# Optimization experiments

Measured on AMD Instinct MI355X. Metric: run time of the kernel, lower is better.

## Reference

```python
import jax, jax.numpy as jnp
import numpy as np

B = 2
N_PER = 100000
M_PER = 27648
C = 32
Z, Y, X = 21, 400, 352
MAX_RANGE = (2, 2, 2)
RADIUS = 8.0
NSAMPLE = 16
VS = np.array([0.2, 0.2, 0.4], np.float32)  # voxel size (x, y, z)


def setup_inputs() -> dict:
    key = jax.random.key(0)
    ks = jax.random.split(key, 6)
    N = B * N_PER
    M = B * M_PER
    space = jnp.array([X * VS[0], Y * VS[1], Z * VS[2]], jnp.float32)
    xyz = jax.random.uniform(ks[0], (N, 3), jnp.float32) * space
    zc = jax.random.randint(ks[1], (M,), 0, Z)
    yc = jax.random.randint(ks[2], (M,), 0, Y)
    xc = jax.random.randint(ks[3], (M,), 0, X)
    bq = jnp.repeat(jnp.arange(B, dtype=jnp.int32), M_PER)
    new_coords = jnp.stack([bq, zc, yc, xc], 1).astype(jnp.int32)
    new_xyz = jnp.stack([(xc + 0.5) * VS[0], (yc + 0.5) * VS[1], (zc + 0.5) * VS[2]], 1).astype(jnp.float32)
    features = jax.random.normal(ks[4], (N, C), jnp.float32)
    raw = jax.random.randint(ks[5], (B, Z, Y, X), -N_PER, N_PER)
    offs = (jnp.arange(B) * N_PER)[:, None, None, None]
    voxel2point_indices = jnp.where(raw < 0, -1, raw + offs).astype(jnp.int32)
    xyz_batch_cnt = jnp.full((B,), N_PER, jnp.int32)
    new_xyz_batch_cnt = jnp.full((B,), M_PER, jnp.int32)
    return dict(new_coords=new_coords, xyz=xyz, xyz_batch_cnt=xyz_batch_cnt,
                new_xyz=new_xyz, new_xyz_batch_cnt=new_xyz_batch_cnt,
                features=features, voxel2point_indices=voxel2point_indices)


def _voxel_query(xyz, new_xyz, new_coords, point_indices):
    """Vectorized equivalent of the CUDA voxel_query kernel.
    Returns (idx (M, nsample) int32 global point indices, empty_ball_mask (M,) bool)."""
    zr, yr, xr = MAX_RANGE
    _, Zg, Yg, Xg = point_indices.shape
    M = new_coords.shape[0]
    dz, dy, dx = jnp.meshgrid(jnp.arange(-zr, zr + 1), jnp.arange(-yr, yr + 1),
                              jnp.arange(-xr, xr + 1), indexing='ij')
    offs = jnp.stack([dz.ravel(), dy.ravel(), dx.ravel()], 1)  # (K,3) in CUDA loop order z,y,x
    nb = new_coords[:, None, 1:4] + offs[None]                 # (M,K,3) candidate voxels
    lim = jnp.array([Zg, Yg, Xg])
    inb = jnp.all((nb >= 0) & (nb < lim), -1)                  # (M,K) in-bounds
    nbc = jnp.clip(nb, 0, lim - 1)
    b = new_coords[:, 0]
    pidx = point_indices[b[:, None], nbc[..., 0], nbc[..., 1], nbc[..., 2]]  # (M,K)
    valid = inb & (pidx >= 0)
    pts = xyz[jnp.maximum(pidx, 0)]                            # (M,K,3)
    d2 = jnp.sum((pts - new_xyz[:, None, :]) ** 2, -1)
    valid = valid & (d2 < RADIUS * RADIUS)
    cnt = jnp.minimum(valid.sum(-1), NSAMPLE)                  # (M,)
    # assign each valid candidate its in-order slot; overflow/invalid go to dump column
    slot = jnp.cumsum(valid, -1) - 1
    slot = jnp.where(valid & (slot < NSAMPLE), slot, NSAMPLE)
    rows = jnp.arange(M)[:, None]
    idx = jnp.zeros((M, NSAMPLE + 1), jnp.int32).at[rows, slot].set(pidx)[:, :NSAMPLE]
    first = idx[:, 0]  # CUDA pre-fills all slots with first found index
    idx = jnp.where(jnp.arange(NSAMPLE)[None, :] < cnt[:, None], idx, first[:, None])
    empty = cnt == 0
    idx = jnp.where(empty[:, None], 0, idx)
    return idx, empty


def reference(new_coords, xyz, xyz_batch_cnt, new_xyz, new_xyz_batch_cnt, features, voxel2point_indices):
    idx, empty = _voxel_query(xyz, new_xyz, new_coords, voxel2point_indices)
    # global -> batch-relative (as in the torch loop), empty balls -> 0 of their batch
    xyz_offs = jnp.concatenate([jnp.zeros(1, jnp.int32), jnp.cumsum(xyz_batch_cnt)[:-1].astype(jnp.int32)])
    qb = new_coords[:, 0]
    idx_rel = jnp.where(empty[:, None], 0, idx - xyz_offs[qb][:, None])
    # grouping_operation (stack version): gather with batch offset added back
    gidx = idx_rel + xyz_offs[qb][:, None]                     # (M, nsample) global indices
    grouped_xyz = jnp.transpose(xyz[gidx], (0, 2, 1))          # (M, 3, nsample)
    grouped_features = jnp.transpose(features[gidx], (0, 2, 1))  # (M, C, nsample)
    return grouped_features, grouped_xyz, empty
```

## Files before the change

kernel.cpp:

```cpp
#include <hip/hip_runtime.h>


constexpr int ZG = 21;
constexpr int YG = 400;
constexpr int XG = 352;
constexpr int NS = 16;
constexpr int CF = 32;
constexpr float R2 = 64.0f;

typedef float v4f __attribute__((ext_vector_type(4)));

struct QState {
    int  cnt;
    int  boff;
    int  gfin;
};

__global__ __launch_bounds__(256) void vqg_kernel(
    const int*   __restrict__ new_coords,
    const float* __restrict__ xyz,
    const int*   __restrict__ xyz_batch_cnt,
    const float* __restrict__ new_xyz,
    const float* __restrict__ features,
    const int*   __restrict__ v2p,
    float* __restrict__ out_feat,
    float* __restrict__ out_xyz,
    float* __restrict__ out_empty,
    int M)
{
    const int lane = threadIdx.x & 63;
    const int w    = (blockIdx.x * 256 + threadIdx.x) >> 6;
    const int m0   = w * 2;
    const int m1   = m0 + 1;
    if (m0 >= M) return;
    const bool has1 = (m1 < M);

    const int4 qc0 = *reinterpret_cast<const int4*>(new_coords + (size_t)m0 * 4);
    const int4 qc1 = has1 ? *reinterpret_cast<const int4*>(new_coords + (size_t)m1 * 4) : qc0;
    const float qx0 = new_xyz[m0 * 3 + 0], qy0 = new_xyz[m0 * 3 + 1], qz0 = new_xyz[m0 * 3 + 2];
    const float qx1 = has1 ? new_xyz[m1 * 3 + 0] : 0.f;
    const float qy1 = has1 ? new_xyz[m1 * 3 + 1] : 0.f;
    const float qz1 = has1 ? new_xyz[m1 * 3 + 2] : 0.f;

    int boff0 = 0, boff1 = 0;
    for (int i = 0; i < qc0.x; ++i) boff0 += xyz_batch_cnt[i];
    for (int i = 0; i < qc1.x; ++i) boff1 += xyz_batch_cnt[i];

    const int n0 = lane;
    const int n1 = 64 + lane;
    const int dz0 = n0 / 25 - 2, dy0 = (n0 / 5) % 5 - 2, dx0 = n0 % 5 - 2;
    const int dz1 = n1 / 25 - 2, dy1 = (n1 / 5) % 5 - 2, dx1 = n1 % 5 - 2;
    const bool in1 = (n1 < 125);

    const int* __restrict__ gb0 = v2p + (size_t)qc0.x * (ZG * YG * XG);
    const int* __restrict__ gb1 = v2p + (size_t)qc1.x * (ZG * YG * XG);

    int pa0 = -1, pa1 = -1, pb0 = -1, pb1 = -1;
    {
        const int z = qc0.y + dz0, y = qc0.z + dy0, x = qc0.w + dx0;
        if ((unsigned)z < (unsigned)ZG && (unsigned)y < (unsigned)YG && (unsigned)x < (unsigned)XG)
            pa0 = gb0[((size_t)z * YG + y) * XG + x];
    }
    {
        const int z = qc0.y + dz1, y = qc0.z + dy1, x = qc0.w + dx1;
        if (in1 && (unsigned)z < (unsigned)ZG && (unsigned)y < (unsigned)YG && (unsigned)x < (unsigned)XG)
            pa1 = gb0[((size_t)z * YG + y) * XG + x];
    }
    if (has1) {
        const int z = qc1.y + dz0, y = qc1.z + dy0, x = qc1.w + dx0;
        if ((unsigned)z < (unsigned)ZG && (unsigned)y < (unsigned)YG && (unsigned)x < (unsigned)XG)
            pb0 = gb1[((size_t)z * YG + y) * XG + x];
    }
    if (has1) {
        const int z = qc1.y + dz1, y = qc1.z + dy1, x = qc1.w + dx1;
        if (in1 && (unsigned)z < (unsigned)ZG && (unsigned)y < (unsigned)YG && (unsigned)x < (unsigned)XG)
            pb1 = gb1[((size_t)z * YG + y) * XG + x];
    }

    float a0x = 0, a0y = 0, a0z = 0, a1x = 0, a1y = 0, a1z = 0;
    float b0x = 0, b0y = 0, b0z = 0, b1x = 0, b1y = 0, b1z = 0;
    if (pa0 >= 0) { const float* p = xyz + (size_t)pa0 * 3; a0x = p[0]; a0y = p[1]; a0z = p[2]; }
    if (pa1 >= 0) { const float* p = xyz + (size_t)pa1 * 3; a1x = p[0]; a1y = p[1]; a1z = p[2]; }
    if (pb0 >= 0) { const float* p = xyz + (size_t)pb0 * 3; b0x = p[0]; b0y = p[1]; b0z = p[2]; }
    if (pb1 >= 0) { const float* p = xyz + (size_t)pb1 * 3; b1x = p[0]; b1y = p[1]; b1z = p[2]; }

    bool va0 = false, va1 = false, vb0 = false, vb1 = false;
    if (pa0 >= 0) {
        const float dx = a0x - qx0, dy = a0y - qy0, dz = a0z - qz0;
        va0 = __fadd_rn(__fadd_rn(__fmul_rn(dx, dx), __fmul_rn(dy, dy)), __fmul_rn(dz, dz)) < R2;
    }
    if (pa1 >= 0) {
        const float dx = a1x - qx0, dy = a1y - qy0, dz = a1z - qz0;
        va1 = __fadd_rn(__fadd_rn(__fmul_rn(dx, dx), __fmul_rn(dy, dy)), __fmul_rn(dz, dz)) < R2;
    }
    if (pb0 >= 0) {
        const float dx = b0x - qx1, dy = b0y - qy1, dz = b0z - qz1;
        vb0 = __fadd_rn(__fadd_rn(__fmul_rn(dx, dx), __fmul_rn(dy, dy)), __fmul_rn(dz, dz)) < R2;
    }
    if (pb1 >= 0) {
        const float dx = b1x - qx1, dy = b1y - qy1, dz = b1z - qz1;
        vb1 = __fadd_rn(__fadd_rn(__fmul_rn(dx, dx), __fmul_rn(dy, dy)), __fmul_rn(dz, dz)) < R2;
    }

    const unsigned long long below = (1ull << lane) - 1ull;
    const int junk = (16 + (lane & 31)) << 2;

    int cnt0, gfin0;
    {
        const unsigned long long bal0 = __ballot(va0);
        const unsigned long long bal1 = __ballot(va1);
        const int c0   = (int)__popcll(bal0);
        cnt0 = c0 + (int)__popcll(bal1);
        const int pos0 = (int)__popcll(bal0 & below);
        const int pos1 = c0 + (int)__popcll(bal1 & below);
        const int addr0 = (va0 && pos0 < NS) ? (pos0 << 2) : junk;
        const int addr1 = (va1 && pos1 < NS) ? (pos1 << 2) : junk;
        const int perm0 = __builtin_amdgcn_ds_permute(addr0, pa0);
        const int perm1 = __builtin_amdgcn_ds_permute(addr1, pa1);
        const int sel   = (lane < c0) ? perm0 : perm1;
        const int first = __shfl(sel, 0);
        const int c16   = cnt0 < NS ? cnt0 : NS;
        gfin0 = (cnt0 == 0) ? boff0 : (((lane & 15) < c16) ? sel : first);
    }
    int cnt1 = 0, gfin1 = 0;
    if (has1) {
        const unsigned long long bal0 = __ballot(vb0);
        const unsigned long long bal1 = __ballot(vb1);
        const int c0   = (int)__popcll(bal0);
        cnt1 = c0 + (int)__popcll(bal1);
        const int pos0 = (int)__popcll(bal0 & below);
        const int pos1 = c0 + (int)__popcll(bal1 & below);
        const int addr0 = (vb0 && pos0 < NS) ? (pos0 << 2) : junk;
        const int addr1 = (vb1 && pos1 < NS) ? (pos1 << 2) : junk;
        const int perm0 = __builtin_amdgcn_ds_permute(addr0, pb0);
        const int perm1 = __builtin_amdgcn_ds_permute(addr1, pb1);
        const int sel   = (lane < c0) ? perm0 : perm1;
        const int first = __shfl(sel, 0);
        const int c16   = cnt1 < NS ? cnt1 : NS;
        gfin1 = (cnt1 == 0) ? boff1 : (((lane & 15) < c16) ? sel : first);
    }

    const int s0lane = (lane & 3) << 2;
    const int a_r0 = __shfl(gfin0, s0lane + 0);
    const int a_r1 = __shfl(gfin0, s0lane + 1);
    const int a_r2 = __shfl(gfin0, s0lane + 2);
    const int a_r3 = __shfl(gfin0, s0lane + 3);
    const int b_r0 = __shfl(gfin1, s0lane + 0);
    const int b_r1 = __shfl(gfin1, s0lane + 1);
    const int b_r2 = __shfl(gfin1, s0lane + 2);
    const int b_r3 = __shfl(gfin1, s0lane + 3);

    {
        const int s = lane & 15;
        const int d = lane >> 4;
        if (lane < 48) {
            const int row = __shfl(gfin0, s);
            __builtin_nontemporal_store(xyz[(size_t)row * 3 + d],
                                        out_xyz + (size_t)m0 * 48 + d * 16 + s);
        }
        if (lane == 0)
            __builtin_nontemporal_store(cnt0 == 0 ? 1.0f : 0.0f, out_empty + m0);
        if (has1) {
            if (lane < 48) {
                const int row = __shfl(gfin1, s);
                __builtin_nontemporal_store(xyz[(size_t)row * 3 + d],
                                            out_xyz + (size_t)m1 * 48 + d * 16 + s);
            }
            if (lane == 0)
                __builtin_nontemporal_store(cnt1 == 0 ? 1.0f : 0.0f, out_empty + m1);
        }
    }

    float* __restrict__ of0 = out_feat + (size_t)m0 * (CF * NS);
    float* __restrict__ of1 = out_feat + (size_t)m1 * (CF * NS);
    #pragma unroll
    for (int k = 0; k < 2; ++k) {
        const int c = k * 16 + (lane >> 2);
        v4f v;
        v[0] = features[(size_t)a_r0 * CF + c];
        v[1] = features[(size_t)a_r1 * CF + c];
        v[2] = features[(size_t)a_r2 * CF + c];
        v[3] = features[(size_t)a_r3 * CF + c];
        __builtin_nontemporal_store(v, reinterpret_cast<v4f*>(of0 + k * 256 + (lane << 2)));
    }
    if (has1) {
        #pragma unroll
        for (int k = 0; k < 2; ++k) {
            const int c = k * 16 + (lane >> 2);
            v4f v;
            v[0] = features[(size_t)b_r0 * CF + c];
            v[1] = features[(size_t)b_r1 * CF + c];
            v[2] = features[(size_t)b_r2 * CF + c];
            v[3] = features[(size_t)b_r3 * CF + c];
            __builtin_nontemporal_store(v, reinterpret_cast<v4f*>(of1 + k * 256 + (lane << 2)));
        }
    }
}

extern "C" void kernel_launch(void* const* d_in, const int* in_sizes, int n_in,
                              void* d_out, int out_size, void* d_ws, size_t ws_size,
                              hipStream_t stream) {
    const int*   new_coords    = (const int*)d_in[0];
    const float* xyz           = (const float*)d_in[1];
    const int*   xyz_batch_cnt = (const int*)d_in[2];
    const float* new_xyz       = (const float*)d_in[3];
    const float* features      = (const float*)d_in[5];
    const int*   v2p           = (const int*)d_in[6];

    const int M = in_sizes[0] / 4;

    float* out_feat  = (float*)d_out;
    float* out_xyz   = out_feat + (size_t)M * CF * NS;
    float* out_empty = out_xyz + (size_t)M * 3 * NS;

    const int waves  = (M + 1) / 2;
    const int blocks = (waves + 3) / 4;
    vqg_kernel<<<blocks, 256, 0, stream>>>(
        new_coords, xyz, xyz_batch_cnt, new_xyz, features, v2p,
        out_feat, out_xyz, out_empty, M);
}
```

Before: 53.43 us.

## Convert to persistent grid-stride waves with software-prefetched voxel lookups

Switches from one wave per query pair to a fixed grid of 8192 waves that loop over pairs with a stride. While the current pair is processed, the next pair's descriptors and its voxel-grid indices are loaded, so the dependent gather chain overlaps with the previous pair's work. The aim is to hide the latency of the v2p -> xyz -> features load chain, at the cost of more live registers and less wave-level parallelism, since there are about 27.6k pairs for 8192 waves.

```diff
diff --git a/kernel.cpp b/kernel.cpp
--- a/kernel.cpp
+++ b/kernel.cpp
@@ -10,10 +10,11 @@
 
 typedef float v4f __attribute__((ext_vector_type(4)));
 
-struct QState {
-    int  cnt;
-    int  boff;
-    int  gfin;
+struct PairDesc {
+    int4  qc0, qc1;
+    float qx0, qy0, qz0, qx1, qy1, qz1;
+    int   boff0, boff1;
+    bool  has1;
 };
 
 __global__ __launch_bounds__(256) void vqg_kernel(
@@ -26,174 +27,199 @@
     float* __restrict__ out_feat,
     float* __restrict__ out_xyz,
     float* __restrict__ out_empty,
-    int M)
+    int M, int nwaves)
 {
     const int lane = threadIdx.x & 63;
     const int w    = (blockIdx.x * 256 + threadIdx.x) >> 6;
-    const int m0   = w * 2;
-    const int m1   = m0 + 1;
-    if (m0 >= M) return;
-    const bool has1 = (m1 < M);
-
-    const int4 qc0 = *reinterpret_cast<const int4*>(new_coords + (size_t)m0 * 4);
-    const int4 qc1 = has1 ? *reinterpret_cast<const int4*>(new_coords + (size_t)m1 * 4) : qc0;
-    const float qx0 = new_xyz[m0 * 3 + 0], qy0 = new_xyz[m0 * 3 + 1], qz0 = new_xyz[m0 * 3 + 2];
-    const float qx1 = has1 ? new_xyz[m1 * 3 + 0] : 0.f;
-    const float qy1 = has1 ? new_xyz[m1 * 3 + 1] : 0.f;
-    const float qz1 = has1 ? new_xyz[m1 * 3 + 2] : 0.f;
-
-    int boff0 = 0, boff1 = 0;
-    for (int i = 0; i < qc0.x; ++i) boff0 += xyz_batch_cnt[i];
-    for (int i = 0; i < qc1.x; ++i) boff1 += xyz_batch_cnt[i];
-
-    const int n0 = lane;
+    const int npairs = (M + 1) / 2;
+    int slot = w;
+    if (slot >= npairs) return;
+
     const int n1 = 64 + lane;
-    const int dz0 = n0 / 25 - 2, dy0 = (n0 / 5) % 5 - 2, dx0 = n0 % 5 - 2;
-    const int dz1 = n1 / 25 - 2, dy1 = (n1 / 5) % 5 - 2, dx1 = n1 % 5 - 2;
+    const int dz0 = lane / 25 - 2, dy0 = (lane / 5) % 5 - 2, dx0 = lane % 5 - 2;
+    const int dz1 = n1 / 25 - 2,   dy1 = (n1 / 5) % 5 - 2,   dx1 = n1 % 5 - 2;
     const bool in1 = (n1 < 125);
-
-    const int* __restrict__ gb0 = v2p + (size_t)qc0.x * (ZG * YG * XG);
-    const int* __restrict__ gb1 = v2p + (size_t)qc1.x * (ZG * YG * XG);
-
-    int pa0 = -1, pa1 = -1, pb0 = -1, pb1 = -1;
-    {
-        const int z = qc0.y + dz0, y = qc0.z + dy0, x = qc0.w + dx0;
-        if ((unsigned)z < (unsigned)ZG && (unsigned)y < (unsigned)YG && (unsigned)x < (unsigned)XG)
-            pa0 = gb0[((size_t)z * YG + y) * XG + x];
-    }
-    {
-        const int z = qc0.y + dz1, y = qc0.z + dy1, x = qc0.w + dx1;
-        if (in1 && (unsigned)z < (unsigned)ZG && (unsigned)y < (unsigned)YG && (unsigned)x < (unsigned)XG)
-            pa1 = gb0[((size_t)z * YG + y) * XG + x];
-    }
-    if (has1) {
-        const int z = qc1.y + dz0, y = qc1.z + dy0, x = qc1.w + dx0;
-        if ((unsigned)z < (unsigned)ZG && (unsigned)y < (unsigned)YG && (unsigned)x < (unsigned)XG)
-            pb0 = gb1[((size_t)z * YG + y) * XG + x];
-    }
-    if (has1) {
-        const int z = qc1.y + dz1, y = qc1.z + dy1, x = qc1.w + dx1;
-        if (in1 && (unsigned)z < (unsigned)ZG && (unsigned)y < (unsigned)YG && (unsigned)x < (unsigned)XG)
-            pb1 = gb1[((size_t)z * YG + y) * XG + x];
-    }
-
-    float a0x = 0, a0y = 0, a0z = 0, a1x = 0, a1y = 0, a1z = 0;
-    float b0x = 0, b0y = 0, b0z = 0, b1x = 0, b1y = 0, b1z = 0;
-    if (pa0 >= 0) { const float* p = xyz + (size_t)pa0 * 3; a0x = p[0]; a0y = p[1]; a0z = p[2]; }
-    if (pa1 >= 0) { const float* p = xyz + (size_t)pa1 * 3; a1x = p[0]; a1y = p[1]; a1z = p[2]; }
-    if (pb0 >= 0) { const float* p = xyz + (size_t)pb0 * 3; b0x = p[0]; b0y = p[1]; b0z = p[2]; }
-    if (pb1 >= 0) { const float* p = xyz + (size_t)pb1 * 3; b1x = p[0]; b1y = p[1]; b1z = p[2]; }
-
-    bool va0 = false, va1 = false, vb0 = false, vb1 = false;
-    if (pa0 >= 0) {
-        const float dx = a0x - qx0, dy = a0y - qy0, dz = a0z - qz0;
-        va0 = __fadd_rn(__fadd_rn(__fmul_rn(dx, dx), __fmul_rn(dy, dy)), __fmul_rn(dz, dz)) < R2;
-    }
-    if (pa1 >= 0) {
-        const float dx = a1x - qx0, dy = a1y - qy0, dz = a1z - qz0;
-        va1 = __fadd_rn(__fadd_rn(__fmul_rn(dx, dx), __fmul_rn(dy, dy)), __fmul_rn(dz, dz)) < R2;
-    }
-    if (pb0 >= 0) {
-        const float dx = b0x - qx1, dy = b0y - qy1, dz = b0z - qz1;
-        vb0 = __fadd_rn(__fadd_rn(__fmul_rn(dx, dx), __fmul_rn(dy, dy)), __fmul_rn(dz, dz)) < R2;
-    }
-    if (pb1 >= 0) {
-        const float dx = b1x - qx1, dy = b1y - qy1, dz = b1z - qz1;
-        vb1 = __fadd_rn(__fadd_rn(__fmul_rn(dx, dx), __fmul_rn(dy, dy)), __fmul_rn(dz, dz)) < R2;
-    }
-
     const unsigned long long below = (1ull << lane) - 1ull;
     const int junk = (16 + (lane & 31)) << 2;
 
-    int cnt0, gfin0;
-    {
-        const unsigned long long bal0 = __ballot(va0);
-        const unsigned long long bal1 = __ballot(va1);
-        const int c0   = (int)__popcll(bal0);
-        cnt0 = c0 + (int)__popcll(bal1);
-        const int pos0 = (int)__popcll(bal0 & below);
-        const int pos1 = c0 + (int)__popcll(bal1 & below);
-        const int addr0 = (va0 && pos0 < NS) ? (pos0 << 2) : junk;
-        const int addr1 = (va1 && pos1 < NS) ? (pos1 << 2) : junk;
-        const int perm0 = __builtin_amdgcn_ds_permute(addr0, pa0);
-        const int perm1 = __builtin_amdgcn_ds_permute(addr1, pa1);
-        const int sel   = (lane < c0) ? perm0 : perm1;
-        const int first = __shfl(sel, 0);
-        const int c16   = cnt0 < NS ? cnt0 : NS;
-        gfin0 = (cnt0 == 0) ? boff0 : (((lane & 15) < c16) ? sel : first);
-    }
-    int cnt1 = 0, gfin1 = 0;
-    if (has1) {
-        const unsigned long long bal0 = __ballot(vb0);
-        const unsigned long long bal1 = __ballot(vb1);
-        const int c0   = (int)__popcll(bal0);
-        cnt1 = c0 + (int)__popcll(bal1);
-        const int pos0 = (int)__popcll(bal0 & below);
-        const int pos1 = c0 + (int)__popcll(bal1 & below);
-        const int addr0 = (vb0 && pos0 < NS) ? (pos0 << 2) : junk;
-        const int addr1 = (vb1 && pos1 < NS) ? (pos1 << 2) : junk;
-        const int perm0 = __builtin_amdgcn_ds_permute(addr0, pb0);
-        const int perm1 = __builtin_amdgcn_ds_permute(addr1, pb1);
-        const int sel   = (lane < c0) ? perm0 : perm1;
-        const int first = __shfl(sel, 0);
-        const int c16   = cnt1 < NS ? cnt1 : NS;
-        gfin1 = (cnt1 == 0) ? boff1 : (((lane & 15) < c16) ? sel : first);
-    }
-
-    const int s0lane = (lane & 3) << 2;
-    const int a_r0 = __shfl(gfin0, s0lane + 0);
-    const int a_r1 = __shfl(gfin0, s0lane + 1);
-    const int a_r2 = __shfl(gfin0, s0lane + 2);
-    const int a_r3 = __shfl(gfin0, s0lane + 3);
-    const int b_r0 = __shfl(gfin1, s0lane + 0);
-    const int b_r1 = __shfl(gfin1, s0lane + 1);
-    const int b_r2 = __shfl(gfin1, s0lane + 2);
-    const int b_r3 = __shfl(gfin1, s0lane + 3);
-
-    {
-        const int s = lane & 15;
-        const int d = lane >> 4;
-        if (lane < 48) {
-            const int row = __shfl(gfin0, s);
-            __builtin_nontemporal_store(xyz[(size_t)row * 3 + d],
-                                        out_xyz + (size_t)m0 * 48 + d * 16 + s);
-        }
-        if (lane == 0)
-            __builtin_nontemporal_store(cnt0 == 0 ? 1.0f : 0.0f, out_empty + m0);
+    auto load_desc = [&](int s, PairDesc& d) {
+        const int m0 = s * 2, m1 = m0 + 1;
+        d.has1 = (m1 < M);
+        d.qc0 = *reinterpret_cast<const int4*>(new_coords + (size_t)m0 * 4);
+        d.qc1 = d.has1 ? *reinterpret_cast<const int4*>(new_coords + (size_t)m1 * 4) : d.qc0;
+        d.qx0 = new_xyz[m0 * 3 + 0]; d.qy0 = new_xyz[m0 * 3 + 1]; d.qz0 = new_xyz[m0 * 3 + 2];
+        d.qx1 = d.has1 ? new_xyz[m1 * 3 + 0] : 0.f;
+        d.qy1 = d.has1 ? new_xyz[m1 * 3 + 1] : 0.f;
+        d.qz1 = d.has1 ? new_xyz[m1 * 3 + 2] : 0.f;
+        int b0 = 0, b1 = 0;
+        for (int i = 0; i < d.qc0.x; ++i) b0 += xyz_batch_cnt[i];
+        for (int i = 0; i < d.qc1.x; ++i) b1 += xyz_batch_cnt[i];
+        d.boff0 = b0; d.boff1 = b1;
+    };
+    auto load_v2p = [&](const PairDesc& d, int& pa0, int& pa1, int& pb0, int& pb1) {
+        const int* __restrict__ gb0 = v2p + (size_t)d.qc0.x * (ZG * YG * XG);
+        const int* __restrict__ gb1 = v2p + (size_t)d.qc1.x * (ZG * YG * XG);
+        pa0 = -1; pa1 = -1; pb0 = -1; pb1 = -1;
+        {
+            const int z = d.qc0.y + dz0, y = d.qc0.z + dy0, x = d.qc0.w + dx0;
+            if ((unsigned)z < (unsigned)ZG && (unsigned)y < (unsigned)YG && (unsigned)x < (unsigned)XG)
+                pa0 = gb0[((size_t)z * YG + y) * XG + x];
+        }
+        {
+            const int z = d.qc0.y + dz1, y = d.qc0.z + dy1, x = d.qc0.w + dx1;
+            if (in1 && (unsigned)z < (unsigned)ZG && (unsigned)y < (unsigned)YG && (unsigned)x < (unsigned)XG)
+                pa1 = gb0[((size_t)z * YG + y) * XG + x];
+        }
+        if (d.has1) {
+            const int z = d.qc1.y + dz0, y = d.qc1.z + dy0, x = d.qc1.w + dx0;
+            if ((unsigned)z < (unsigned)ZG && (unsigned)y < (unsigned)YG && (unsigned)x < (unsigned)XG)
+                pb0 = gb1[((size_t)z * YG + y) * XG + x];
+        }
+        if (d.has1) {
+            const int z = d.qc1.y + dz1, y = d.qc1.z + dy1, x = d.qc1.w + dx1;
+            if (in1 && (unsigned)z < (unsigned)ZG && (unsigned)y < (unsigned)YG && (unsigned)x < (unsigned)XG)
+                pb1 = gb1[((size_t)z * YG + y) * XG + x];
+        }
+    };
+
+    PairDesc cur;
+    int pa0, pa1, pb0, pb1;
+    load_desc(slot, cur);
+    load_v2p(cur, pa0, pa1, pb0, pb1);
+
+    for (;;) {
+        const int m0 = slot * 2, m1 = m0 + 1;
+        const bool has1 = cur.has1;
+
+        float a0x = 0, a0y = 0, a0z = 0, a1x = 0, a1y = 0, a1z = 0;
+        float b0x = 0, b0y = 0, b0z = 0, b1x = 0, b1y = 0, b1z = 0;
+        if (pa0 >= 0) { const float* p = xyz + (size_t)pa0 * 3; a0x = p[0]; a0y = p[1]; a0z = p[2]; }
+        if (pa1 >= 0) { const float* p = xyz + (size_t)pa1 * 3; a1x = p[0]; a1y = p[1]; a1z = p[2]; }
+        if (pb0 >= 0) { const float* p = xyz + (size_t)pb0 * 3; b0x = p[0]; b0y = p[1]; b0z = p[2]; }
+        if (pb1 >= 0) { const float* p = xyz + (size_t)pb1 * 3; b1x = p[0]; b1y = p[1]; b1z = p[2]; }
+
+        const int nslot = slot + nwaves;
+        const bool hasnext = (nslot < npairs);
+        PairDesc nxt;
+        int na0 = -1, na1 = -1, nb0 = -1, nb1 = -1;
+        if (hasnext) {
+            load_desc(nslot, nxt);
+            load_v2p(nxt, na0, na1, nb0, nb1);
+        }
+
+        bool va0 = false, va1 = false, vb0 = false, vb1 = false;
+        if (pa0 >= 0) {
+            const float dx = a0x - cur.qx0, dy = a0y - cur.qy0, dz = a0z - cur.qz0;
+            va0 = __fadd_rn(__fadd_rn(__fmul_rn(dx, dx), __fmul_rn(dy, dy)), __fmul_rn(dz, dz)) < R2;
+        }
+        if (pa1 >= 0) {
+            const float dx = a1x - cur.qx0, dy = a1y - cur.qy0, dz = a1z - cur.qz0;
+            va1 = __fadd_rn(__fadd_rn(__fmul_rn(dx, dx), __fmul_rn(dy, dy)), __fmul_rn(dz, dz)) < R2;
+        }
+        if (pb0 >= 0) {
+            const float dx = b0x - cur.qx1, dy = b0y - cur.qy1, dz = b0z - cur.qz1;
+            vb0 = __fadd_rn(__fadd_rn(__fmul_rn(dx, dx), __fmul_rn(dy, dy)), __fmul_rn(dz, dz)) < R2;
+        }
+        if (pb1 >= 0) {
+            const float dx = b1x - cur.qx1, dy = b1y - cur.qy1, dz = b1z - cur.qz1;
+            vb1 = __fadd_rn(__fadd_rn(__fmul_rn(dx, dx), __fmul_rn(dy, dy)), __fmul_rn(dz, dz)) < R2;
+        }
+
+        int cnt0, gfin0;
+        {
+            const unsigned long long bal0 = __ballot(va0);
+            const unsigned long long bal1 = __ballot(va1);
+            const int c0   = (int)__popcll(bal0);
+            cnt0 = c0 + (int)__popcll(bal1);
+            const int pos0 = (int)__popcll(bal0 & below);
+            const int pos1 = c0 + (int)__popcll(bal1 & below);
+            const int addr0 = (va0 && pos0 < NS) ? (pos0 << 2) : junk;
+            const int addr1 = (va1 && pos1 < NS) ? (pos1 << 2) : junk;
+            const int perm0 = __builtin_amdgcn_ds_permute(addr0, pa0);
+            const int perm1 = __builtin_amdgcn_ds_permute(addr1, pa1);
+            const int sel   = (lane < c0) ? perm0 : perm1;
+            const int first = __shfl(sel, 0);
+            const int c16   = cnt0 < NS ? cnt0 : NS;
+            gfin0 = (cnt0 == 0) ? cur.boff0 : (((lane & 15) < c16) ? sel : first);
+        }
+        int cnt1 = 0, gfin1 = 0;
         if (has1) {
+            const unsigned long long bal0 = __ballot(vb0);
+            const unsigned long long bal1 = __ballot(vb1);
+            const int c0   = (int)__popcll(bal0);
+            cnt1 = c0 + (int)__popcll(bal1);
+            const int pos0 = (int)__popcll(bal0 & below);
+            const int pos1 = c0 + (int)__popcll(bal1 & below);
+            const int addr0 = (vb0 && pos0 < NS) ? (pos0 << 2) : junk;
+            const int addr1 = (vb1 && pos1 < NS) ? (pos1 << 2) : junk;
+            const int perm0 = __builtin_amdgcn_ds_permute(addr0, pb0);
+            const int perm1 = __builtin_amdgcn_ds_permute(addr1, pb1);
+            const int sel   = (lane < c0) ? perm0 : perm1;
+            const int first = __shfl(sel, 0);
+            const int c16   = cnt1 < NS ? cnt1 : NS;
+            gfin1 = (cnt1 == 0) ? cur.boff1 : (((lane & 15) < c16) ? sel : first);
+        }
+
+        {
+            const int s = lane & 15;
+            const int d = lane >> 4;
             if (lane < 48) {
-                const int row = __shfl(gfin1, s);
+                const int row = __shfl(gfin0, s);
                 __builtin_nontemporal_store(xyz[(size_t)row * 3 + d],
-                                            out_xyz + (size_t)m1 * 48 + d * 16 + s);
+                                            out_xyz + (size_t)m0 * 48 + d * 16 + s);
             }
             if (lane == 0)
-                __builtin_nontemporal_store(cnt1 == 0 ? 1.0f : 0.0f, out_empty + m1);
-        }
-    }
-
-    float* __restrict__ of0 = out_feat + (size_t)m0 * (CF * NS);
-    float* __restrict__ of1 = out_feat + (size_t)m1 * (CF * NS);
-    #pragma unroll
-    for (int k = 0; k < 2; ++k) {
-        const int c = k * 16 + (lane >> 2);
-        v4f v;
-        v[0] = features[(size_t)a_r0 * CF + c];
-        v[1] = features[(size_t)a_r1 * CF + c];
-        v[2] = features[(size_t)a_r2 * CF + c];
-        v[3] = features[(size_t)a_r3 * CF + c];
-        __builtin_nontemporal_store(v, reinterpret_cast<v4f*>(of0 + k * 256 + (lane << 2)));
-    }
-    if (has1) {
+                __builtin_nontemporal_store(cnt0 == 0 ? 1.0f : 0.0f, out_empty + m0);
+            if (has1) {
+                if (lane < 48) {
+                    const int row = __shfl(gfin1, s);
+                    __builtin_nontemporal_store(xyz[(size_t)row * 3 + d],
+                                                out_xyz + (size_t)m1 * 48 + d * 16 + s);
+                }
+                if (lane == 0)
+                    __builtin_nontemporal_store(cnt1 == 0 ? 1.0f : 0.0f, out_empty + m1);
+            }
+        }
+
+        const int s0lane = (lane & 3) << 2;
+        const int a_r0 = __shfl(gfin0, s0lane + 0);
+        const int a_r1 = __shfl(gfin0, s0lane + 1);
+        const int a_r2 = __shfl(gfin0, s0lane + 2);
+        const int a_r3 = __shfl(gfin0, s0lane + 3);
+        const int b_r0 = __shfl(gfin1, s0lane + 0);
+        const int b_r1 = __shfl(gfin1, s0lane + 1);
+        const int b_r2 = __shfl(gfin1, s0lane + 2);
+        const int b_r3 = __shfl(gfin1, s0lane + 3);
+
+        float* __restrict__ of0 = out_feat + (size_t)m0 * (CF * NS);
+        float* __restrict__ of1 = out_feat + (size_t)m1 * (CF * NS);
         #pragma unroll
         for (int k = 0; k < 2; ++k) {
             const int c = k * 16 + (lane >> 2);
             v4f v;
-            v[0] = features[(size_t)b_r0 * CF + c];
-            v[1] = features[(size_t)b_r1 * CF + c];
-            v[2] = features[(size_t)b_r2 * CF + c];
-            v[3] = features[(size_t)b_r3 * CF + c];
-            __builtin_nontemporal_store(v, reinterpret_cast<v4f*>(of1 + k * 256 + (lane << 2)));
-        }
+            v[0] = features[(size_t)a_r0 * CF + c];
+            v[1] = features[(size_t)a_r1 * CF + c];
+            v[2] = features[(size_t)a_r2 * CF + c];
+            v[3] = features[(size_t)a_r3 * CF + c];
+            __builtin_nontemporal_store(v, reinterpret_cast<v4f*>(of0 + k * 256 + (lane << 2)));
+        }
+        if (has1) {
+            #pragma unroll
+            for (int k = 0; k < 2; ++k) {
+                const int c = k * 16 + (lane >> 2);
+                v4f v;
+                v[0] = features[(size_t)b_r0 * CF + c];
+                v[1] = features[(size_t)b_r1 * CF + c];
+                v[2] = features[(size_t)b_r2 * CF + c];
+                v[3] = features[(size_t)b_r3 * CF + c];
+                __builtin_nontemporal_store(v, reinterpret_cast<v4f*>(of1 + k * 256 + (lane << 2)));
+            }
+        }
+
+        if (!hasnext) break;
+        cur = nxt;
+        pa0 = na0; pa1 = na1; pb0 = nb0; pb1 = nb1;
+        slot = nslot;
     }
 }
 
@@ -213,9 +239,12 @@
     float* out_xyz   = out_feat + (size_t)M * CF * NS;
     float* out_empty = out_xyz + (size_t)M * 3 * NS;
 
-    const int waves  = (M + 1) / 2;
-    const int blocks = (waves + 3) / 4;
+    const int npairs = (M + 1) / 2;
+    const int nwaves = 8192;
+    int blocks = (nwaves * 64) / 256;
+    const int needed = (npairs + 3) / 4;
+    if (blocks > needed) blocks = needed;
     vqg_kernel<<<blocks, 256, 0, stream>>>(
         new_coords, xyz, xyz_batch_cnt, new_xyz, features, v2p,
-        out_feat, out_xyz, out_empty, M);
+        out_feat, out_xyz, out_empty, M, blocks * 4);
 }
```

After: 130.8 us. +144.8%, slower.
